# Kernel optimization log

Measured on AMD Instinct MI355X. Metric: run time of the kernel, lower is better.

Reference implementation:

```python
import jax, jax.numpy as jnp
import numpy as np

T = 8
TAU = 2.0       # spikingjelly LIFNode default tau
VTH = 1.0       # default v_threshold
ALPHA = 2.0     # surrogate.ATan alpha
EPS = 1e-5      # BatchNorm eps


@jax.custom_vjp
def spike_fn(x):
    # Heaviside with ATan surrogate gradient
    return (x >= 0.0).astype(x.dtype)

def _spike_fwd(x):
    return (x >= 0.0).astype(x.dtype), x

def _spike_bwd(x, g):
    sg = (ALPHA / 2.0) / (1.0 + (jnp.pi / 2.0 * ALPHA * x) ** 2)
    return (g * sg,)

spike_fn.defvjp(_spike_fwd, _spike_bwd)


def lif(x_seq):
    """Multi-step LIF over leading time axis. decay_input=True, hard reset to 0, detach_reset."""
    def step(v, x):
        v = v + (x - v) / TAU            # charge
        s = spike_fn(v - VTH)            # fire (surrogate grad)
        v = v * (1.0 - jax.lax.stop_gradient(s))  # detached hard reset to v_reset=0
        return v, s
    _, s_seq = jax.lax.scan(step, jnp.zeros_like(x_seq[0]), x_seq)
    return s_seq


def conv2d(x, w, b, stride):
    y = jax.lax.conv_general_dilated(x, w, (stride, stride), 'VALID',
                                     dimension_numbers=('NCHW', 'OIHW', 'NCHW'))
    return y + b[None, :, None, None]


def batchnorm(x, g, b):
    # training-mode BN over merged (T*B, H, W) axes, matching step_mode='m' BatchNorm2d
    m = x.mean((0, 2, 3), keepdims=True)
    v = x.var((0, 2, 3), keepdims=True)
    return g[None, :, None, None] * (x - m) * jax.lax.rsqrt(v + EPS) + b[None, :, None, None]


def setup_inputs() -> dict:
    key = jax.random.key(0)
    ks = jax.random.split(key, 12)
    def w_init(k, shape):
        fan_in = int(np.prod(shape[1:]))
        return jax.random.normal(k, shape, dtype=jnp.float32) / np.sqrt(fan_in)
    x = jax.random.normal(ks[0], (128, 4, 84, 84), dtype=jnp.float32)
    return {
        'x': x,
        'conv1_w': w_init(ks[1], (32, 4, 8, 8)),  'conv1_b': jnp.zeros((32,), jnp.float32),
        'bn1_g': jnp.ones((32,), jnp.float32),    'bn1_b': jnp.zeros((32,), jnp.float32),
        'conv2_w': w_init(ks[2], (64, 32, 4, 4)), 'conv2_b': jnp.zeros((64,), jnp.float32),
        'bn2_g': jnp.ones((64,), jnp.float32),    'bn2_b': jnp.zeros((64,), jnp.float32),
        'conv3_w': w_init(ks[3], (64, 64, 3, 3)), 'conv3_b': jnp.zeros((64,), jnp.float32),
        'bn3_g': jnp.ones((64,), jnp.float32),    'bn3_b': jnp.zeros((64,), jnp.float32),
        'fc1_w': w_init(ks[4], (512, 3136)),      'fc1_b': jnp.zeros((512,), jnp.float32),
        'fco_w': w_init(ks[5], (2, 512)),         'fco_b': jnp.zeros((2,), jnp.float32),
    }


def reference(x, conv1_w, conv1_b, bn1_g, bn1_b, conv2_w, conv2_b, bn2_g, bn2_b,
              conv3_w, conv3_b, bn3_g, bn3_b, fc1_w, fc1_b, fco_w, fco_b):
    B = x.shape[0]
    # replicate input over T timesteps; fold T into batch for conv/BN (step_mode='m')
    xs = jnp.broadcast_to(x, (T,) + x.shape).reshape((T * B,) + x.shape[1:])

    h = batchnorm(conv2d(xs, conv1_w, conv1_b, 4), bn1_g, bn1_b)   # [TB,32,20,20]
    s = lif(h.reshape((T, B) + h.shape[1:]))
    h = s.reshape((T * B,) + s.shape[2:])

    h = batchnorm(conv2d(h, conv2_w, conv2_b, 2), bn2_g, bn2_b)    # [TB,64,9,9]
    s = lif(h.reshape((T, B) + h.shape[1:]))
    h = s.reshape((T * B,) + s.shape[2:])

    h = batchnorm(conv2d(h, conv3_w, conv3_b, 1), bn3_g, bn3_b)    # [TB,64,7,7]
    s = lif(h.reshape((T, B) + h.shape[1:]))                        # [T,B,64,7,7]

    feat = s.reshape(T, B, -1)                                      # [T,B,3136]
    hid = lif(jnp.einsum('tbi,oi->tbo', feat, fc1_w) + fc1_b)       # [T,B,512]
    out_seq = jnp.einsum('tbo,ko->tbk', hid, fco_w) + fco_b         # [T,B,2]
    return out_seq.mean(0)                                          # [B,2]
```

## Files before the change

kernel.cpp:

```cpp
#include <hip/hip_runtime.h>
#include <cstdint>
#include <cstddef>

#define TT 8

#define E2_ELEMS (128*64*81)
#define E3_ELEMS (128*64*49)

typedef __attribute__((ext_vector_type(8))) short short8;
typedef __attribute__((ext_vector_type(4))) float f32x4;

__global__ void prep_all(const float* __restrict__ w1, const float* __restrict__ w2,
                         const float* __restrict__ w3, float* __restrict__ wT1,
                         __bf16* __restrict__ w2f, __bf16* __restrict__ w3f) {
  int i = blockIdx.x * 256 + threadIdx.x;
  if (i < 8192) {
    int oc = i >> 8, pos = i & 255;
    wT1[(oc >> 4) * 4096 + pos * 16 + (oc & 15)] = w1[oc * 256 + pos];
  } else if (i < 106496) {
    int v = i - 8192;
    int j    = v & 7;
    int oc   = (v >> 3) & 63;
    int quad = (v >> 9) & 3;
    int ksg  = (v >> 11) & 15;
    int term = v >> 15;
    int k = ksg * 32 + quad * 8 + j;
    int ci = k >> 4, kpos = k & 15;
    float w = w2[oc * 512 + ci * 16 + kpos];
    float hf = (float)(__bf16)w;
    float r1 = w - hf;
    float mf = (float)(__bf16)r1;
    float r2 = r1 - mf;
    w2f[v] = (term == 0) ? (__bf16)w : (term == 1) ? (__bf16)r1 : (__bf16)r2;
  } else if (i < 217088) {
    int v = i - 106496;
    int j    = v & 7;
    int oc   = (v >> 3) & 63;
    int quad = (v >> 9) & 3;
    int tk   = v >> 11;
    int term = tk / 18, kstep = tk % 18;
    int k = kstep * 32 + quad * 8 + j;
    int pos = k >> 6, ci = k & 63;
    float w = w3[oc * 576 + ci * 9 + pos];
    float hf = (float)(__bf16)w;
    float r1 = w - hf;
    float mf = (float)(__bf16)r1;
    float r2 = r1 - mf;
    w3f[v] = (term == 0) ? (__bf16)w : (term == 1) ? (__bf16)r1 : (__bf16)r2;
  }
}

__global__ __launch_bounds__(256) void prep_wff(const float* __restrict__ w,
                                                __bf16* __restrict__ wf) {
  __shared__ float tile[12544];
  int oc0 = blockIdx.x * 32;
  int ci0 = blockIdx.y * 8;
  int tid = threadIdx.x;
  for (int f = tid; f < 12544; f += 256) {
    int oc_l = f / 392, r = f - oc_l * 392;
    tile[f] = w[(size_t)(oc0 + oc_l) * 3136 + ci0 * 49 + r];
  }
  __syncthreads();
  int squad = (ci0 & 31) >> 3;
  int sadd  = ci0 >> 5;
  for (int g = tid; g < 1568; g += 256) {
    int pos = g >> 5, oc_l = g & 31;
    union { __bf16 h[8]; uint4 u; } T0, T1, T2;
    #pragma unroll
    for (int j = 0; j < 8; j++) {
      float wv = tile[oc_l * 392 + j * 49 + pos];
      float hf = (float)(__bf16)wv;
      float r1 = wv - hf;
      float mf = (float)(__bf16)r1;
      float r2 = r1 - mf;
      T0.h[j] = (__bf16)wv; T1.h[j] = (__bf16)r1; T2.h[j] = (__bf16)r2;
    }
    int s = pos * 2 + sadd;
    size_t b0 = (((size_t)s * 4 + squad) * 512 + oc0 + oc_l) * 8;
    *(uint4*)(wf + b0)               = T0.u;
    *(uint4*)(wf + b0 + 1605632)     = T1.u;
    *(uint4*)(wf + b0 + 3211264)     = T2.u;
  }
}

__global__ __launch_bounds__(128) void k_conv1(const float* __restrict__ x,
                                               const float* __restrict__ wT,
                                               const float* __restrict__ bias,
                                               float* __restrict__ out,
                                               float* __restrict__ pout) {
  __shared__ float xt[8064];
  int tid = threadIdx.x;
  int img = blockIdx.x >> 2;
  int q   = blockIdx.x & 3;
  int och = blockIdx.y;
  float4* dst = (float4*)xt;
  #pragma unroll
  for (int ci = 0; ci < 4; ci++) {
    const float4* s4 = (const float4*)(x + (size_t)img * 28224 + ci * 7056 + q * 1680);
    for (int i = tid; i < 504; i += 128) dst[ci * 504 + i] = s4[i];
  }
  __syncthreads();
  bool active = tid < 100;
  int oyl = tid / 20, ox = tid % 20;
  float acc[16];
  #pragma unroll
  for (int j = 0; j < 16; j++) acc[j] = 0.f;
  if (active) {
    int xb0 = oyl * 336 + ox * 4;
    const float* wh = wT + och * 4096;
    #pragma unroll 1
    for (int ci = 0; ci < 4; ci++) {
      #pragma unroll 1
      for (int ky = 0; ky < 8; ky++) {
        const float* xr = xt + ci * 2016 + xb0 + ky * 84;
        float4 xa  = *(const float4*)xr;
        float4 xbv = *(const float4*)(xr + 4);
        const float* wr = wh + (ci * 8 + ky) * 128;
        float xs[8] = {xa.x, xa.y, xa.z, xa.w, xbv.x, xbv.y, xbv.z, xbv.w};
        #pragma unroll
        for (int kx = 0; kx < 8; kx++) {
          #pragma unroll
          for (int j = 0; j < 16; j++)
            acc[j] = fmaf(xs[kx], wr[kx * 16 + j], acc[j]);
        }
      }
    }
  }
  __syncthreads();
  size_t obase = (size_t)img * 12800 + och * 6400 + (q * 5 + oyl) * 20 + ox;
  #pragma unroll
  for (int j = 0; j < 16; j++) {
    float v = 0.f;
    if (active) {
      v = acc[j] + bias[och * 16 + j];
      out[obase + j * 400] = v;
    }
    xt[j * 128 + tid] = v;
    xt[2048 + j * 128 + tid] = v * v;
  }
  __syncthreads();
  for (int off = 64; off > 0; off >>= 1) {
    if (tid < off) {
      #pragma unroll
      for (int j = 0; j < 16; j++) {
        xt[j * 128 + tid] += xt[j * 128 + tid + off];
        xt[2048 + j * 128 + tid] += xt[2048 + j * 128 + tid + off];
      }
    }
    __syncthreads();
  }
  if (tid < 16) {
    pout[(och * 16 + tid) * 512 + blockIdx.x] = xt[tid * 128];
    pout[16384 + (och * 16 + tid) * 512 + blockIdx.x] = xt[2048 + tid * 128];
  }
}

__global__ void k_bnfinal2(const float* __restrict__ pin, int sqoff, float n,
                           float* __restrict__ meanArr, float* __restrict__ rstdArr) {
  __shared__ float l0[256], l1[256];
  int c = blockIdx.x, tid = threadIdx.x;
  l0[tid] = pin[c * 512 + tid] + pin[c * 512 + tid + 256];
  l1[tid] = pin[sqoff + c * 512 + tid] + pin[sqoff + c * 512 + tid + 256];
  __syncthreads();
  for (int k = 128; k > 0; k >>= 1) {
    if (tid < k) { l0[tid] += l0[tid + k]; l1[tid] += l1[tid + k]; }
    __syncthreads();
  }
  if (tid == 0) {
    float m = l0[0] / n;
    float var = l1[0] / n - m * m;
    meanArr[c] = m;
    rstdArr[c] = rsqrtf(var + 1e-5f);
  }
}

__global__ void k_lif1b(const float* __restrict__ h, const float* __restrict__ mean,
                        const float* __restrict__ rstd, const float* __restrict__ g,
                        const float* __restrict__ bb, uint32_t* __restrict__ sout) {
  int idx = blockIdx.x * 256 + threadIdx.x;
  int ic = idx / 20;
  int ci = ic & 31;
  const float* hp = h + (size_t)idx * 20;
  float gm = g[ci], mm = mean[ci], rs = rstd[ci], bc = bb[ci];
  float xv[20];
  #pragma unroll
  for (int j4 = 0; j4 < 5; j4++) {
    float4 hv = ((const float4*)hp)[j4];
    xv[j4 * 4 + 0] = gm * (hv.x - mm) * rs + bc;
    xv[j4 * 4 + 1] = gm * (hv.y - mm) * rs + bc;
    xv[j4 * 4 + 2] = gm * (hv.z - mm) * rs + bc;
    xv[j4 * 4 + 3] = gm * (hv.w - mm) * rs + bc;
  }
  float v[20];
  #pragma unroll
  for (int j = 0; j < 20; j++) v[j] = 0.f;
  #pragma unroll
  for (int t = 0; t < TT; t++) {
    uint32_t w = 0;
    #pragma unroll
    for (int j = 0; j < 20; j++) {
      v[j] = v[j] + (xv[j] - v[j]) * 0.5f;
      uint32_t s = (v[j] >= 1.0f);
      w |= s << j;
      if (s) v[j] = 0.f;
    }
    sout[t * 81920 + idx] = w;
  }
}

template <int W, int NROW>
__global__ void k_lifb(const float* __restrict__ h, const float* __restrict__ mean,
                       const float* __restrict__ rstd, const float* __restrict__ g,
                       const float* __restrict__ bb, uint32_t* __restrict__ sout,
                       int E) {
  int idx = blockIdx.x * 256 + threadIdx.x;
  int bc = idx / NROW;
  int c = bc & 63;
  float gm = g[c], mm = mean[c], rs = rstd[c], bcn = bb[c];
  float v[W];
  #pragma unroll
  for (int j = 0; j < W; j++) v[j] = 0.f;
  int nword = 128 * 64 * NROW;
  #pragma unroll
  for (int t = 0; t < TT; t++) {
    const float* hp = h + (size_t)t * E + (size_t)idx * W;
    uint32_t w = 0;
    #pragma unroll
    for (int j = 0; j < W; j++) {
      float xv = gm * (hp[j] - mm) * rs + bcn;
      v[j] = v[j] + (xv - v[j]) * 0.5f;
      uint32_t s = (v[j] >= 1.0f);
      w |= s << j;
      if (s) v[j] = 0.f;
    }
    sout[t * nword + idx] = w;
  }
}

__global__ __launch_bounds__(256) void k_conv2m(const uint32_t* __restrict__ s1b,
                                                const __bf16* __restrict__ wf,
                                                const float* __restrict__ bias,
                                                float* __restrict__ out,
                                                float* __restrict__ pout) {
  __shared__ uint32_t sp[1280];
  __shared__ uint4 wl4[3072];
  __bf16* wl = (__bf16*)wl4;
  int tid = threadIdx.x;
  int img0 = blockIdx.x * 2;
  {
    const uint32_t* src = s1b + (size_t)img0 * 640;
    for (int i = tid; i < 1280; i += 256) sp[i] = src[i];
  }
  int wave = tid >> 6, lane = tid & 63;
  int img_local = wave >> 1;
  int tg = wave & 1;
  int l15 = lane & 15, quad = lane >> 4;
  int ci_off = quad >> 1;
  int kyp = (quad & 1) * 2;
  int spb[3], sh[3];
  #pragma unroll
  for (int mt = 0; mt < 3; mt++) {
    int px = tg * 48 + mt * 16 + l15;
    if (px > 80) px = 80;
    int oy = px / 9, ox = px - oy * 9;
    sh[mt]  = ox * 2;
    spb[mt] = img_local * 640 + ci_off * 20 + oy * 2 + kyp;
  }
  f32x4 acc[3][4];
  #pragma unroll
  for (int mt = 0; mt < 3; mt++)
    #pragma unroll
    for (int nt = 0; nt < 4; nt++) acc[mt][nt] = (f32x4){0.f, 0.f, 0.f, 0.f};

  for (int kc = 0; kc < 4; kc++) {
    __syncthreads();
    for (int o = tid * 8; o < 24576; o += 2048) {
      int tk = o >> 11;
      int term = tk >> 2, ksl = tk & 3;
      const __bf16* src = wf + (((term * 16 + kc * 4 + ksl)) << 11) + (o & 2047);
      *(uint4*)(wl + o) = *(const uint4*)src;
    }
    __syncthreads();
    #pragma unroll
    for (int ks = 0; ks < 4; ks++) {
      int ksg = kc * 4 + ks;
      short8 a[3];
      #pragma unroll
      for (int mt = 0; mt < 3; mt++) {
        uint32_t w0 = sp[spb[mt] + ksg * 40];
        uint32_t w1 = sp[spb[mt] + ksg * 40 + 1];
        uint32_t n0 = (w0 >> sh[mt]) & 15u;
        uint32_t n1 = (w1 >> sh[mt]) & 15u;
        union { uint32_t u[4]; short8 v; } A;
        A.u[0] = ((n0 & 1u) ? 0x3F80u : 0u) | ((n0 & 2u) ? 0x3F800000u : 0u);
        A.u[1] = ((n0 & 4u) ? 0x3F80u : 0u) | ((n0 & 8u) ? 0x3F800000u : 0u);
        A.u[2] = ((n1 & 1u) ? 0x3F80u : 0u) | ((n1 & 2u) ? 0x3F800000u : 0u);
        A.u[3] = ((n1 & 4u) ? 0x3F80u : 0u) | ((n1 & 8u) ? 0x3F800000u : 0u);
        a[mt] = A.v;
      }
      #pragma unroll
      for (int term = 0; term < 3; term++) {
        int fb = ((term * 4 + ks) << 11) + (quad << 9);
        #pragma unroll
        for (int nt = 0; nt < 4; nt++) {
          short8 b = *(const short8*)(wl + fb + ((nt << 4) + l15) * 8);
          #pragma unroll
          for (int mt = 0; mt < 3; mt++)
            acc[mt][nt] = __builtin_amdgcn_mfma_f32_16x16x32_bf16(a[mt], b, acc[mt][nt], 0, 0, 0);
        }
      }
    }
  }
  float sl[4], sl2[4];
  #pragma unroll
  for (int nt = 0; nt < 4; nt++) {
    sl[nt] = 0.f; sl2[nt] = 0.f;
    int oc = nt * 16 + l15;
    float bv = bias[oc];
    float* op = out + ((size_t)(img0 + img_local) * 64 + oc) * 81;
    #pragma unroll
    for (int mt = 0; mt < 3; mt++) {
      int pxr = tg * 48 + mt * 16 + quad * 4;
      #pragma unroll
      for (int r = 0; r < 4; r++) {
        int px = pxr + r;
        if (px < 81) {
          float v = acc[mt][nt][r] + bv;
          op[px] = v;
          sl[nt] += v; sl2[nt] += v * v;
        }
      }
    }
  }
  __syncthreads();
  float* sred = (float*)wl4;
  #pragma unroll
  for (int nt = 0; nt < 4; nt++) {
    int idx = (nt * 16 + l15) * 16 + (wave * 4 + quad);
    sred[idx] = sl[nt];
    sred[1024 + idx] = sl2[nt];
  }
  __syncthreads();
  if (tid < 64) {
    float s = 0.f, s2 = 0.f;
    #pragma unroll
    for (int k = 0; k < 16; k++) { s += sred[tid * 16 + k]; s2 += sred[1024 + tid * 16 + k]; }
    pout[tid * 512 + blockIdx.x] = s;
    pout[32768 + tid * 512 + blockIdx.x] = s2;
  }
}

__global__ void k_s2T(const uint32_t* __restrict__ sbits, uint32_t* __restrict__ s2T) {
  __shared__ uint32_t sb[576];
  int n = blockIdx.x;
  int t = n >> 7, b = n & 127;
  int tid = threadIdx.x;
  const uint32_t* src = sbits + t * 73728 + b * 576;
  for (int i = tid; i < 576; i += 256) sb[i] = src[i];
  __syncthreads();
  if (tid >= 162) return;
  int half = tid & 1, pc = tid >> 1;
  int r = pc / 9, cpix = pc - r * 9;
  uint32_t w = 0;
  #pragma unroll
  for (int ci = 0; ci < 32; ci++)
    w |= (((sb[(half * 32 + ci) * 9 + r] >> cpix) & 1u) << ci);
  s2T[(size_t)n * 162 + pc * 2 + half] = w;
}

__global__ __launch_bounds__(256) void k_conv3m(const uint32_t* __restrict__ s2T,
                                                const __bf16* __restrict__ wf,
                                                const float* __restrict__ bias,
                                                float* __restrict__ out,
                                                float* __restrict__ pout) {
  __shared__ uint32_t sp[324];
  __shared__ uint4 wl4[4608];
  __bf16* wl = (__bf16*)wl4;
  int tid = threadIdx.x;
  int img0 = blockIdx.x * 2;
  {
    const uint32_t* src = s2T + (size_t)img0 * 162;
    for (int i = tid; i < 324; i += 256) sp[i] = src[i];
  }
  int wave = tid >> 6, lane = tid & 63;
  int img_local = wave >> 1, tg = wave & 1;
  int l15 = lane & 15, quad = lane >> 4;
  int qsh = quad * 8;
  int base[2];
  #pragma unroll
  for (int mt = 0; mt < 2; mt++) {
    int px = tg * 32 + mt * 16 + l15;
    if (px > 48) px = 48;
    int oy = px / 7, ox = px - oy * 7;
    base[mt] = img_local * 162 + (oy * 9 + ox) * 2;
  }
  f32x4 acc[2][4];
  #pragma unroll
  for (int mt = 0; mt < 2; mt++)
    #pragma unroll
    for (int nt = 0; nt < 4; nt++) acc[mt][nt] = (f32x4){0.f, 0.f, 0.f, 0.f};

  #pragma unroll
  for (int kc = 0; kc < 3; kc++) {
    __syncthreads();
    #pragma unroll
    for (int it = 0; it < 18; it++) {
      const __bf16* s = wf + (((it / 6) * 18 + kc * 6 + (it % 6)) << 11) + tid * 8;
      *(uint4*)(wl + (it << 11) + tid * 8) = *(const uint4*)s;
    }
    __syncthreads();
    #pragma unroll
    for (int ksl = 0; ksl < 6; ksl++) {
      int kstep = kc * 6 + ksl;
      int pos = kstep >> 1, cihalf = kstep & 1;
      int ky = pos / 3, kx = pos % 3;
      short8 a[2];
      #pragma unroll
      for (int mt = 0; mt < 2; mt++) {
        uint32_t word = sp[base[mt] + (ky * 9 + kx) * 2 + cihalf];
        uint32_t byt = (word >> qsh) & 255u;
        union { uint32_t u[4]; short8 v; } A;
        A.u[0] = ((byt & 1u)  ? 0x3F80u : 0u) | ((byt & 2u)   ? 0x3F800000u : 0u);
        A.u[1] = ((byt & 4u)  ? 0x3F80u : 0u) | ((byt & 8u)   ? 0x3F800000u : 0u);
        A.u[2] = ((byt & 16u) ? 0x3F80u : 0u) | ((byt & 32u)  ? 0x3F800000u : 0u);
        A.u[3] = ((byt & 64u) ? 0x3F80u : 0u) | ((byt & 128u) ? 0x3F800000u : 0u);
        a[mt] = A.v;
      }
      #pragma unroll
      for (int term = 0; term < 3; term++) {
        int fb = ((term * 6 + ksl) << 11) + (quad << 9);
        #pragma unroll
        for (int nt = 0; nt < 4; nt++) {
          short8 b = *(const short8*)(wl + fb + ((nt << 4) + l15) * 8);
          #pragma unroll
          for (int mt = 0; mt < 2; mt++)
            acc[mt][nt] = __builtin_amdgcn_mfma_f32_16x16x32_bf16(a[mt], b, acc[mt][nt], 0, 0, 0);
        }
      }
    }
  }
  float sl[4], sl2[4];
  #pragma unroll
  for (int nt = 0; nt < 4; nt++) {
    sl[nt] = 0.f; sl2[nt] = 0.f;
    int oc = nt * 16 + l15;
    float bv = bias[oc];
    float* op = out + ((size_t)(img0 + img_local) * 64 + oc) * 49;
    #pragma unroll
    for (int mt = 0; mt < 2; mt++) {
      int pxr = tg * 32 + mt * 16 + quad * 4;
      #pragma unroll
      for (int r = 0; r < 4; r++) {
        int px = pxr + r;
        if (px < 49) {
          float v = acc[mt][nt][r] + bv;
          op[px] = v;
          sl[nt] += v; sl2[nt] += v * v;
        }
      }
    }
  }
  __syncthreads();
  float* sred = (float*)wl4;
  #pragma unroll
  for (int nt = 0; nt < 4; nt++) {
    int idx = (nt * 16 + l15) * 16 + (wave * 4 + quad);
    sred[idx] = sl[nt];
    sred[1024 + idx] = sl2[nt];
  }
  __syncthreads();
  if (tid < 64) {
    float s = 0.f, s2 = 0.f;
    #pragma unroll
    for (int k = 0; k < 16; k++) { s += sred[tid * 16 + k]; s2 += sred[1024 + tid * 16 + k]; }
    pout[tid * 512 + blockIdx.x] = s;
    pout[32768 + tid * 512 + blockIdx.x] = s2;
  }
}

__global__ void k_s3T(const uint32_t* __restrict__ sbits, uint32_t* __restrict__ s3T) {
  __shared__ uint32_t sb[896];
  int r0 = blockIdx.x * 2;
  int tid = threadIdx.x;
  for (int i = tid; i < 896; i += 256) {
    int rl = i / 448, o = i - rl * 448;
    int row = r0 + rl;
    sb[i] = sbits[(row >> 7) * 57344 + (row & 127) * 448 + o];
  }
  __syncthreads();
  if (tid >= 196) return;
  int rl = tid / 98, k = tid - rl * 98;
  int pos = k >> 1, half = k & 1;
  int py = pos / 7, px = pos - py * 7;
  const uint32_t* base = sb + rl * 448 + half * 224 + py;
  uint32_t w = 0;
  #pragma unroll
  for (int ci = 0; ci < 32; ci++)
    w |= ((base[ci * 7] >> px) & 1u) << ci;
  s3T[(size_t)(r0 + rl) * 98 + k] = w;
}

__global__ __launch_bounds__(256) void k_fc1m(const uint32_t* __restrict__ s3T,
                                              const __bf16* __restrict__ wf,
                                              float* __restrict__ part) {
  __shared__ uint32_t aS[6272];
  int tid = threadIdx.x;
  int row0 = blockIdx.x * 64;
  int oc0  = blockIdx.y * 32;
  {
    const uint32_t* src = s3T + (size_t)row0 * 98;
    for (int i = tid; i < 6272; i += 256) aS[i] = src[i];
  }
  __syncthreads();
  int wave = tid >> 6, lane = tid & 63;
  int l15 = lane & 15, quad = lane >> 4;
  int qsh = quad * 8;
  f32x4 acc[4][2];
  #pragma unroll
  for (int mt = 0; mt < 4; mt++)
    #pragma unroll
    for (int nt = 0; nt < 2; nt++) acc[mt][nt] = (f32x4){0.f, 0.f, 0.f, 0.f};
  int nIter = (wave < 2) ? 25 : 24;
  #pragma unroll 1
  for (int i = 0; i < nIter; i++) {
    int ks = i * 4 + wave;
    short8 a[4];
    #pragma unroll
    for (int mt = 0; mt < 4; mt++) {
      uint32_t word = aS[(mt * 16 + l15) * 98 + ks];
      uint32_t byt = (word >> qsh) & 255u;
      union { uint32_t u[4]; short8 v; } A;
      A.u[0] = ((byt & 1u)  ? 0x3F80u : 0u) | ((byt & 2u)   ? 0x3F800000u : 0u);
      A.u[1] = ((byt & 4u)  ? 0x3F80u : 0u) | ((byt & 8u)   ? 0x3F800000u : 0u);
      A.u[2] = ((byt & 16u) ? 0x3F80u : 0u) | ((byt & 32u)  ? 0x3F800000u : 0u);
      A.u[3] = ((byt & 64u) ? 0x3F80u : 0u) | ((byt & 128u) ? 0x3F800000u : 0u);
      a[mt] = A.v;
    }
    #pragma unroll
    for (int term = 0; term < 3; term++) {
      size_t fb = ((size_t)((term * 98 + ks) * 4 + quad) * 512 + oc0 + l15) * 8;
      #pragma unroll
      for (int nt = 0; nt < 2; nt++) {
        short8 b = *(const short8*)(wf + fb + nt * 128);
        #pragma unroll
        for (int mt = 0; mt < 4; mt++)
          acc[mt][nt] = __builtin_amdgcn_mfma_f32_16x16x32_bf16(a[mt], b, acc[mt][nt], 0, 0, 0);
      }
    }
  }
  #pragma unroll
  for (int mt = 0; mt < 4; mt++) {
    #pragma unroll
    for (int nt = 0; nt < 2; nt++) {
      int oc = oc0 + nt * 16 + l15;
      #pragma unroll
      for (int r = 0; r < 4; r++) {
        int row = row0 + mt * 16 + quad * 4 + r;
        part[(size_t)wave * 524288 + (size_t)row * 512 + oc] = acc[mt][nt][r];
      }
    }
  }
}

__global__ void k_fc1red_lif(const float* __restrict__ part, const float* __restrict__ bias,
                             unsigned char* __restrict__ hid) {
  int idx = blockIdx.x * 256 + threadIdx.x;
  float bv = bias[idx & 511];
  float v = 0.f;
  #pragma unroll
  for (int t = 0; t < TT; t++) {
    float a = part[t * 65536 + idx];
    #pragma unroll
    for (int j = 1; j < 4; j++) a += part[(size_t)j * 524288 + t * 65536 + idx];
    a += bv;
    v = v + (a - v) * 0.5f;
    unsigned char s = (v >= 1.0f);
    hid[t * 65536 + idx] = s;
    if (s) v = 0.f;
  }
}

__global__ void k_fco(const unsigned char* __restrict__ hid, const float* __restrict__ w,
                      const float* __restrict__ bias, float* __restrict__ out) {
  int b = blockIdx.x, tid = threadIdx.x;
  float a0 = 0.f, a1 = 0.f;
  for (int t = 0; t < TT; t++) {
    const unsigned char* hrow = hid + ((size_t)t * 128 + b) * 512;
    for (int o = tid; o < 512; o += 256) {
      if (hrow[o]) { a0 += w[o]; a1 += w[512 + o]; }
    }
  }
  __shared__ float l0[256], l1[256];
  l0[tid] = a0; l1[tid] = a1; __syncthreads();
  for (int k = 128; k > 0; k >>= 1) {
    if (tid < k) { l0[tid] += l0[tid + k]; l1[tid] += l1[tid + k]; }
    __syncthreads();
  }
  if (tid == 0) {
    out[b * 2 + 0] = l0[0] * 0.125f + bias[0];
    out[b * 2 + 1] = l1[0] * 0.125f + bias[1];
  }
}

extern "C" void kernel_launch(void* const* d_in, const int* in_sizes, int n_in,
                              void* d_out, int out_size, void* d_ws, size_t ws_size,
                              hipStream_t stream) {
  const float* x    = (const float*)d_in[0];
  const float* c1w  = (const float*)d_in[1];
  const float* c1b  = (const float*)d_in[2];
  const float* bn1g = (const float*)d_in[3];
  const float* bn1b = (const float*)d_in[4];
  const float* c2w  = (const float*)d_in[5];
  const float* c2b  = (const float*)d_in[6];
  const float* bn2g = (const float*)d_in[7];
  const float* bn2b = (const float*)d_in[8];
  const float* c3w  = (const float*)d_in[9];
  const float* c3b  = (const float*)d_in[10];
  const float* bn3g = (const float*)d_in[11];
  const float* bn3b = (const float*)d_in[12];
  const float* fc1w = (const float*)d_in[13];
  const float* fc1b = (const float*)d_in[14];
  const float* fcow = (const float*)d_in[15];
  const float* fcob = (const float*)d_in[16];
  float* out = (float*)d_out;

  char* ws = (char*)d_ws;
  float*    h1     = (float*)(ws + 0);
  uint32_t* s1bits = (uint32_t*)(ws + 6553600);
  float*    h2     = (float*)(ws + 19660800);
  uint32_t* s2bits = (uint32_t*)(ws + 40894464);
  float*    h3     = (float*)(ws + 46202880);
  uint32_t* s3bits = (uint32_t*)(ws + 59047936);
  unsigned char* hid = (unsigned char*)(ws + 64356352);
  float*    st     = (float*)(ws + 64880640);
  __bf16*   w2f  = (__bf16*)(ws + 60882944);
  __bf16*   w3f  = (__bf16*)(ws + 61079552);
  uint32_t* s2T  = (uint32_t*)(ws + 61300736);
  float*    wT1  = (float*)(ws + 62390272);
  float*    bnpart = (float*)(ws + 9437184);
  __bf16*   wff    = (__bf16*)(ws + 19660800);
  float*    f1part = (float*)(ws + 29360128);
  uint32_t* s3T    = (uint32_t*)(ws + 43253760);

  prep_all   <<<848, 256, 0, stream>>>(c1w, c2w, c3w, wT1, w2f, w3f);
  k_conv1    <<<dim3(512, 2), 128, 0, stream>>>(x, wT1, c1b, h1, bnpart);
  k_bnfinal2 <<<32, 256, 0, stream>>>(bnpart, 16384, 51200.f, st, st + 32);
  k_lif1b    <<<320, 256, 0, stream>>>(h1, st, st + 32, bn1g, bn1b, s1bits);

  k_conv2m   <<<512, 256, 0, stream>>>(s1bits, w2f, c2b, h2, bnpart);
  k_bnfinal2 <<<64, 256, 0, stream>>>(bnpart, 32768, 82944.f, st + 64, st + 128);
  k_lifb<9, 9><<<288, 256, 0, stream>>>(h2, st + 64, st + 128, bn2g, bn2b, s2bits, E2_ELEMS);
  prep_wff   <<<dim3(16, 8), 256, 0, stream>>>(fc1w, wff);

  k_s2T      <<<1024, 256, 0, stream>>>(s2bits, s2T);
  k_conv3m   <<<512, 256, 0, stream>>>(s2T, w3f, c3b, h3, bnpart);
  k_bnfinal2 <<<64, 256, 0, stream>>>(bnpart, 32768, 50176.f, st + 192, st + 256);
  k_lifb<7, 7><<<224, 256, 0, stream>>>(h3, st + 192, st + 256, bn3g, bn3b, s3bits, E3_ELEMS);

  k_s3T      <<<512, 256, 0, stream>>>(s3bits, s3T);
  k_fc1m     <<<dim3(16, 16), 256, 0, stream>>>(s3T, wff, f1part);
  k_fc1red_lif<<<256, 256, 0, stream>>>(f1part, fc1b, hid);
  k_fco      <<<128, 256, 0, stream>>>(hid, fcow, fcob, out);
}
```

Before: 260.8 us.

## Fuse LIF with bit transposes and fc1 LIF with output layer; split conv waves by channels

The layer-2 and layer-3 LIF kernels are fused with the bit-transpose kernels, so spike bitmasks go through shared memory straight into the transposed layout and never round-trip through a global intermediate. The fc1 reduction+LIF is fused with the output projection, which removes the hid buffer and one launch. In conv2/conv3 each wave now covers all pixels for half the output channels instead of half the pixels for all channels, which changes the A/B register reuse balance. The workspace is re-laid out to avoid overlap. The fused LIF kernels use only 256 blocks with a serial time loop and barriers, which may lower parallelism.

New measurement: 250.4 us (median of 2 runs). 4.0% less time.

```diff
diff --git a/kernel.cpp b/kernel.cpp
--- a/kernel.cpp
+++ b/kernel.cpp
@@ -77,9 +77,9 @@
     }
     int s = pos * 2 + sadd;
     size_t b0 = (((size_t)s * 4 + squad) * 512 + oc0 + oc_l) * 8;
-    *(uint4*)(wf + b0)               = T0.u;
-    *(uint4*)(wf + b0 + 1605632)     = T1.u;
-    *(uint4*)(wf + b0 + 3211264)     = T2.u;
+    *(uint4*)(wf + b0)           = T0.u;
+    *(uint4*)(wf + b0 + 1605632) = T1.u;
+    *(uint4*)(wf + b0 + 3211264) = T2.u;
   }
 }
 
@@ -208,35 +208,6 @@
   }
 }
 
-template <int W, int NROW>
-__global__ void k_lifb(const float* __restrict__ h, const float* __restrict__ mean,
-                       const float* __restrict__ rstd, const float* __restrict__ g,
-                       const float* __restrict__ bb, uint32_t* __restrict__ sout,
-                       int E) {
-  int idx = blockIdx.x * 256 + threadIdx.x;
-  int bc = idx / NROW;
-  int c = bc & 63;
-  float gm = g[c], mm = mean[c], rs = rstd[c], bcn = bb[c];
-  float v[W];
-  #pragma unroll
-  for (int j = 0; j < W; j++) v[j] = 0.f;
-  int nword = 128 * 64 * NROW;
-  #pragma unroll
-  for (int t = 0; t < TT; t++) {
-    const float* hp = h + (size_t)t * E + (size_t)idx * W;
-    uint32_t w = 0;
-    #pragma unroll
-    for (int j = 0; j < W; j++) {
-      float xv = gm * (hp[j] - mm) * rs + bcn;
-      v[j] = v[j] + (xv - v[j]) * 0.5f;
-      uint32_t s = (v[j] >= 1.0f);
-      w |= s << j;
-      if (s) v[j] = 0.f;
-    }
-    sout[t * nword + idx] = w;
-  }
-}
-
 __global__ __launch_bounds__(256) void k_conv2m(const uint32_t* __restrict__ s1b,
                                                 const __bf16* __restrict__ wf,
                                                 const float* __restrict__ bias,
@@ -253,24 +224,24 @@
   }
   int wave = tid >> 6, lane = tid & 63;
   int img_local = wave >> 1;
-  int tg = wave & 1;
+  int nh = wave & 1;
   int l15 = lane & 15, quad = lane >> 4;
   int ci_off = quad >> 1;
   int kyp = (quad & 1) * 2;
-  int spb[3], sh[3];
-  #pragma unroll
-  for (int mt = 0; mt < 3; mt++) {
-    int px = tg * 48 + mt * 16 + l15;
+  int spb[6], sh[6];
+  #pragma unroll
+  for (int mt = 0; mt < 6; mt++) {
+    int px = mt * 16 + l15;
     if (px > 80) px = 80;
     int oy = px / 9, ox = px - oy * 9;
     sh[mt]  = ox * 2;
     spb[mt] = img_local * 640 + ci_off * 20 + oy * 2 + kyp;
   }
-  f32x4 acc[3][4];
-  #pragma unroll
-  for (int mt = 0; mt < 3; mt++)
-    #pragma unroll
-    for (int nt = 0; nt < 4; nt++) acc[mt][nt] = (f32x4){0.f, 0.f, 0.f, 0.f};
+  f32x4 acc[6][2];
+  #pragma unroll
+  for (int mt = 0; mt < 6; mt++)
+    #pragma unroll
+    for (int nt = 0; nt < 2; nt++) acc[mt][nt] = (f32x4){0.f, 0.f, 0.f, 0.f};
 
   for (int kc = 0; kc < 4; kc++) {
     __syncthreads();
@@ -284,9 +255,9 @@
     #pragma unroll
     for (int ks = 0; ks < 4; ks++) {
       int ksg = kc * 4 + ks;
-      short8 a[3];
-      #pragma unroll
-      for (int mt = 0; mt < 3; mt++) {
+      short8 a[6];
+      #pragma unroll
+      for (int mt = 0; mt < 6; mt++) {
         uint32_t w0 = sp[spb[mt] + ksg * 40];
         uint32_t w1 = sp[spb[mt] + ksg * 40 + 1];
         uint32_t n0 = (w0 >> sh[mt]) & 15u;
@@ -302,25 +273,25 @@
       for (int term = 0; term < 3; term++) {
         int fb = ((term * 4 + ks) << 11) + (quad << 9);
         #pragma unroll
-        for (int nt = 0; nt < 4; nt++) {
-          short8 b = *(const short8*)(wl + fb + ((nt << 4) + l15) * 8);
+        for (int nt = 0; nt < 2; nt++) {
+          short8 b = *(const short8*)(wl + fb + ((((nh << 1) | nt) << 4) + l15) * 8);
           #pragma unroll
-          for (int mt = 0; mt < 3; mt++)
+          for (int mt = 0; mt < 6; mt++)
             acc[mt][nt] = __builtin_amdgcn_mfma_f32_16x16x32_bf16(a[mt], b, acc[mt][nt], 0, 0, 0);
         }
       }
     }
   }
-  float sl[4], sl2[4];
-  #pragma unroll
-  for (int nt = 0; nt < 4; nt++) {
+  float sl[2], sl2[2];
+  #pragma unroll
+  for (int nt = 0; nt < 2; nt++) {
     sl[nt] = 0.f; sl2[nt] = 0.f;
-    int oc = nt * 16 + l15;
+    int oc = nh * 32 + nt * 16 + l15;
     float bv = bias[oc];
     float* op = out + ((size_t)(img0 + img_local) * 64 + oc) * 81;
     #pragma unroll
-    for (int mt = 0; mt < 3; mt++) {
-      int pxr = tg * 48 + mt * 16 + quad * 4;
+    for (int mt = 0; mt < 6; mt++) {
+      int pxr = mt * 16 + quad * 4;
       #pragma unroll
       for (int r = 0; r < 4; r++) {
         int px = pxr + r;
@@ -335,37 +306,79 @@
   __syncthreads();
   float* sred = (float*)wl4;
   #pragma unroll
-  for (int nt = 0; nt < 4; nt++) {
-    int idx = (nt * 16 + l15) * 16 + (wave * 4 + quad);
+  for (int nt = 0; nt < 2; nt++) {
+    int oc = nh * 32 + nt * 16 + l15;
+    int idx = oc * 8 + img_local * 4 + quad;
     sred[idx] = sl[nt];
-    sred[1024 + idx] = sl2[nt];
+    sred[512 + idx] = sl2[nt];
   }
   __syncthreads();
   if (tid < 64) {
     float s = 0.f, s2 = 0.f;
     #pragma unroll
-    for (int k = 0; k < 16; k++) { s += sred[tid * 16 + k]; s2 += sred[1024 + tid * 16 + k]; }
+    for (int k = 0; k < 8; k++) { s += sred[tid * 8 + k]; s2 += sred[512 + tid * 8 + k]; }
     pout[tid * 512 + blockIdx.x] = s;
     pout[32768 + tid * 512 + blockIdx.x] = s2;
   }
 }
 
-__global__ void k_s2T(const uint32_t* __restrict__ sbits, uint32_t* __restrict__ s2T) {
-  __shared__ uint32_t sb[576];
-  int n = blockIdx.x;
-  int t = n >> 7, b = n & 127;
+__global__ __launch_bounds__(256) void k_lifb2T(const float* __restrict__ h,
+                                                const float* __restrict__ mean,
+                                                const float* __restrict__ rstd,
+                                                const float* __restrict__ g,
+                                                const float* __restrict__ bb,
+                                                uint32_t* __restrict__ s2T) {
+  __shared__ uint32_t sb[288];
+  int b = blockIdx.x, half = blockIdx.y;
   int tid = threadIdx.x;
-  const uint32_t* src = sbits + t * 73728 + b * 576;
-  for (int i = tid; i < 576; i += 256) sb[i] = src[i];
-  __syncthreads();
-  if (tid >= 162) return;
-  int half = tid & 1, pc = tid >> 1;
-  int r = pc / 9, cpix = pc - r * 9;
-  uint32_t w = 0;
-  #pragma unroll
-  for (int ci = 0; ci < 32; ci++)
-    w |= (((sb[(half * 32 + ci) * 9 + r] >> cpix) & 1u) << ci);
-  s2T[(size_t)n * 162 + pc * 2 + half] = w;
+  int c1 = half * 32 + tid / 9, py1 = tid % 9;
+  bool has2 = tid < 32;
+  int r2 = tid + 256;
+  int c2i = half * 32 + r2 / 9, py2 = r2 % 9;
+  float gm1 = g[c1], mm1 = mean[c1], rs1 = rstd[c1], bc1 = bb[c1];
+  float gm2 = 0.f, mm2 = 0.f, rs2 = 0.f, bc2 = 0.f;
+  if (has2) { gm2 = g[c2i]; mm2 = mean[c2i]; rs2 = rstd[c2i]; bc2 = bb[c2i]; }
+  float v1[9], v2[9];
+  #pragma unroll
+  for (int j = 0; j < 9; j++) { v1[j] = 0.f; v2[j] = 0.f; }
+  size_t base1 = ((size_t)b * 64 + c1) * 81 + py1 * 9;
+  size_t base2 = has2 ? ((size_t)b * 64 + c2i) * 81 + py2 * 9 : base1;
+  #pragma unroll 1
+  for (int t = 0; t < TT; t++) {
+    const float* hp = h + (size_t)t * E2_ELEMS;
+    uint32_t w = 0;
+    #pragma unroll
+    for (int j = 0; j < 9; j++) {
+      float xv = gm1 * (hp[base1 + j] - mm1) * rs1 + bc1;
+      v1[j] = v1[j] + (xv - v1[j]) * 0.5f;
+      uint32_t s = (v1[j] >= 1.0f);
+      w |= s << j;
+      if (s) v1[j] = 0.f;
+    }
+    sb[tid] = w;
+    if (has2) {
+      uint32_t w2 = 0;
+      #pragma unroll
+      for (int j = 0; j < 9; j++) {
+        float xv = gm2 * (hp[base2 + j] - mm2) * rs2 + bc2;
+        v2[j] = v2[j] + (xv - v2[j]) * 0.5f;
+        uint32_t s = (v2[j] >= 1.0f);
+        w2 |= s << j;
+        if (s) v2[j] = 0.f;
+      }
+      sb[r2] = w2;
+    }
+    __syncthreads();
+    if (tid < 81) {
+      int r = tid / 9, cpix = tid - r * 9;
+      uint32_t wo = 0;
+      #pragma unroll
+      for (int ci = 0; ci < 32; ci++)
+        wo |= ((sb[ci * 9 + r] >> cpix) & 1u) << ci;
+      s2T[(size_t)(t * 128 + b) * 162 + tid * 2 + half] = wo;
+    }
+    __syncthreads();
+  }
 }
 
 __global__ __launch_bounds__(256) void k_conv3m(const uint32_t* __restrict__ s2T,
@@ -383,22 +396,22 @@
     for (int i = tid; i < 324; i += 256) sp[i] = src[i];
   }
   int wave = tid >> 6, lane = tid & 63;
-  int img_local = wave >> 1, tg = wave & 1;
+  int img_local = wave >> 1, nh = wave & 1;
   int l15 = lane & 15, quad = lane >> 4;
   int qsh = quad * 8;
-  int base[2];
-  #pragma unroll
-  for (int mt = 0; mt < 2; mt++) {
-    int px = tg * 32 + mt * 16 + l15;
+  int base[4];
+  #pragma unroll
+  for (int mt = 0; mt < 4; mt++) {
+    int px = mt * 16 + l15;
     if (px > 48) px = 48;
     int oy = px / 7, ox = px - oy * 7;
     base[mt] = img_local * 162 + (oy * 9 + ox) * 2;
   }
-  f32x4 acc[2][4];
-  #pragma unroll
-  for (int mt = 0; mt < 2; mt++)
-    #pragma unroll
-    for (int nt = 0; nt < 4; nt++) acc[mt][nt] = (f32x4){0.f, 0.f, 0.f, 0.f};
+  f32x4 acc[4][2];
+  #pragma unroll
+  for (int mt = 0; mt < 4; mt++)
+    #pragma unroll
+    for (int nt = 0; nt < 2; nt++) acc[mt][nt] = (f32x4){0.f, 0.f, 0.f, 0.f};
 
   #pragma unroll
   for (int kc = 0; kc < 3; kc++) {
@@ -414,9 +427,9 @@
       int kstep = kc * 6 + ksl;
       int pos = kstep >> 1, cihalf = kstep & 1;
       int ky = pos / 3, kx = pos % 3;
-      short8 a[2];
-      #pragma unroll
-      for (int mt = 0; mt < 2; mt++) {
+      short8 a[4];
+      #pragma unroll
+      for (int mt = 0; mt < 4; mt++) {
         uint32_t word = sp[base[mt] + (ky * 9 + kx) * 2 + cihalf];
         uint32_t byt = (word >> qsh) & 255u;
         union { uint32_t u[4]; short8 v; } A;
@@ -430,25 +443,25 @@
       for (int term = 0; term < 3; term++) {
         int fb = ((term * 6 + ksl) << 11) + (quad << 9);
         #pragma unroll
-        for (int nt = 0; nt < 4; nt++) {
-          short8 b = *(const short8*)(wl + fb + ((nt << 4) + l15) * 8);
+        for (int nt = 0; nt < 2; nt++) {
+          short8 b = *(const short8*)(wl + fb + ((((nh << 1) | nt) << 4) + l15) * 8);
           #pragma unroll
-          for (int mt = 0; mt < 2; mt++)
+          for (int mt = 0; mt < 4; mt++)
             acc[mt][nt] = __builtin_amdgcn_mfma_f32_16x16x32_bf16(a[mt], b, acc[mt][nt], 0, 0, 0);
         }
       }
     }
   }
-  float sl[4], sl2[4];
-  #pragma unroll
-  for (int nt = 0; nt < 4; nt++) {
+  float sl[2], sl2[2];
+  #pragma unroll
+  for (int nt = 0; nt < 2; nt++) {
     sl[nt] = 0.f; sl2[nt] = 0.f;
-    int oc = nt * 16 + l15;
+    int oc = nh * 32 + nt * 16 + l15;
     float bv = bias[oc];
     float* op = out + ((size_t)(img0 + img_local) * 64 + oc) * 49;
     #pragma unroll
-    for (int mt = 0; mt < 2; mt++) {
-      int pxr = tg * 32 + mt * 16 + quad * 4;
+    for (int mt = 0; mt < 4; mt++) {
+      int pxr = mt * 16 + quad * 4;
       #pragma unroll
       for (int r = 0; r < 4; r++) {
         int px = pxr + r;
@@ -463,41 +476,65 @@
   __syncthreads();
   float* sred = (float*)wl4;
   #pragma unroll
-  for (int nt = 0; nt < 4; nt++) {
-    int idx = (nt * 16 + l15) * 16 + (wave * 4 + quad);
+  for (int nt = 0; nt < 2; nt++) {
+    int oc = nh * 32 + nt * 16 + l15;
+    int idx = oc * 8 + img_local * 4 + quad;
     sred[idx] = sl[nt];
-    sred[1024 + idx] = sl2[nt];
+    sred[512 + idx] = sl2[nt];
   }
   __syncthreads();
   if (tid < 64) {
     float s = 0.f, s2 = 0.f;
     #pragma unroll
-    for (int k = 0; k < 16; k++) { s += sred[tid * 16 + k]; s2 += sred[1024 + tid * 16 + k]; }
+    for (int k = 0; k < 8; k++) { s += sred[tid * 8 + k]; s2 += sred[512 + tid * 8 + k]; }
     pout[tid * 512 + blockIdx.x] = s;
     pout[32768 + tid * 512 + blockIdx.x] = s2;
   }
 }
 
-__global__ void k_s3T(const uint32_t* __restrict__ sbits, uint32_t* __restrict__ s3T) {
-  __shared__ uint32_t sb[896];
-  int r0 = blockIdx.x * 2;
+__global__ __launch_bounds__(256) void k_lifb3T(const float* __restrict__ h,
+                                                const float* __restrict__ mean,
+                                                const float* __restrict__ rstd,
+                                                const float* __restrict__ g,
+                                                const float* __restrict__ bb,
+                                                uint32_t* __restrict__ s3T) {
+  __shared__ uint32_t sb[224];
+  int b = blockIdx.x, half = blockIdx.y;
   int tid = threadIdx.x;
-  for (int i = tid; i < 896; i += 256) {
-    int rl = i / 448, o = i - rl * 448;
-    int row = r0 + rl;
-    sb[i] = sbits[(row >> 7) * 57344 + (row & 127) * 448 + o];
-  }
-  __syncthreads();
-  if (tid >= 196) return;
-  int rl = tid / 98, k = tid - rl * 98;
-  int pos = k >> 1, half = k & 1;
-  int py = pos / 7, px = pos - py * 7;
-  const uint32_t* base = sb + rl * 448 + half * 224 + py;
-  uint32_t w = 0;
-  #pragma unroll
-  for (int ci = 0; ci < 32; ci++)
-    w |= ((base[ci * 7] >> px) & 1u) << ci;
-  s3T[(size_t)(r0 + rl) * 98 + k] = w;
+  bool active = tid < 224;
+  int row = active ? tid : 0;
+  int c = half * 32 + row / 7, py = row % 7;
+  float gm = g[c], mm = mean[c], rs = rstd[c], bc = bb[c];
+  float v[7];
+  #pragma unroll
+  for (int j = 0; j < 7; j++) v[j] = 0.f;
+  size_t base = ((size_t)b * 64 + c) * 49 + py * 7;
+  #pragma unroll 1
+  for (int t = 0; t < TT; t++) {
+    const float* hp = h + (size_t)t * E3_ELEMS;
+    if (active) {
+      uint32_t w = 0;
+      #pragma unroll
+      for (int j = 0; j < 7; j++) {
+        float xv = gm * (hp[base + j] - mm) * rs + bc;
+        v[j] = v[j] + (xv - v[j]) * 0.5f;
+        uint32_t s = (v[j] >= 1.0f);
+        w |= s << j;
+        if (s) v[j] = 0.f;
+      }
+      sb[tid] = w;
+    }
+    __syncthreads();
+    if (tid < 49) {
+      int py2 = tid / 7, px = tid - py2 * 7;
+      uint32_t wo = 0;
+      #pragma unroll
+      for (int ci = 0; ci < 32; ci++)
+        wo |= ((sb[ci * 7 + py2] >> px) & 1u) << ci;
+      s3T[(size_t)(t * 128 + b) * 98 + tid * 2 + half] = wo;
+    }
+    __syncthreads();
+  }
 }
 
 __global__ __launch_bounds__(256) void k_fc1m(const uint32_t* __restrict__ s3T,
@@ -562,33 +599,36 @@
   }
 }
 
-__global__ void k_fc1red_lif(const float* __restrict__ part, const float* __restrict__ bias,
-                             unsigned char* __restrict__ hid) {
-  int idx = blockIdx.x * 256 + threadIdx.x;
-  float bv = bias[idx & 511];
-  float v = 0.f;
+__global__ __launch_bounds__(256) void k_fc1fco(const float* __restrict__ part,
+                                                const float* __restrict__ bias,
+                                                const float* __restrict__ w,
+                                                const float* __restrict__ fcob,
+                                                float* __restrict__ out) {
+  int b = blockIdx.x, tid = threadIdx.x;
+  int o0 = tid, o1 = tid + 256;
+  float bv0 = bias[o0], bv1 = bias[o1];
+  float v0 = 0.f, v1 = 0.f;
+  float a0 = 0.f, a1 = 0.f;
   #pragma unroll
   for (int t = 0; t < TT; t++) {
-    float a = part[t * 65536 + idx];
-    #pragma unroll
-    for (int j = 1; j < 4; j++) a += part[(size_t)j * 524288 + t * 65536 + idx];
-    a += bv;
-    v = v + (a - v) * 0.5f;
-    unsigned char s = (v >= 1.0f);
-    hid[t * 65536 + idx] = s;
-    if (s) v = 0.f;
-  }
-}
-
-__global__ void k_fco(const unsigned char* __restrict__ hid, const float* __restrict__ w,
-                      const float* __restrict__ bias, float* __restrict__ out) {
-  int b = blockIdx.x, tid = threadIdx.x;
-  float a0 = 0.f, a1 = 0.f;
-  for (int t = 0; t < TT; t++) {
-    const unsigned char* hrow = hid + ((size_t)t * 128 + b) * 512;
-    for (int o = tid; o < 512; o += 256) {
-      if (hrow[o]) { a0 += w[o]; a1 += w[512 + o]; }
-    }
+    int idx0 = t * 65536 + b * 512 + o0;
+    float s0 = part[idx0];
+    #pragma unroll
+    for (int j = 1; j < 4; j++) s0 += part[(size_t)j * 524288 + idx0];
+    s0 += bv0;
+    v0 = v0 + (s0 - v0) * 0.5f;
+    bool sp0 = (v0 >= 1.0f);
+    if (sp0) v0 = 0.f;
+    int idx1 = idx0 + 256;
+    float s1 = part[idx1];
+    #pragma unroll
+    for (int j = 1; j < 4; j++) s1 += part[(size_t)j * 524288 + idx1];
+    s1 += bv1;
+    v1 = v1 + (s1 - v1) * 0.5f;
+    bool sp1 = (v1 >= 1.0f);
+    if (sp1) v1 = 0.f;
+    if (sp0) { a0 += w[o0]; a1 += w[512 + o0]; }
+    if (sp1) { a0 += w[o1]; a1 += w[512 + o1]; }
   }
   __shared__ float l0[256], l1[256];
   l0[tid] = a0; l1[tid] = a1; __syncthreads();
@@ -597,8 +637,8 @@
     __syncthreads();
   }
   if (tid == 0) {
-    out[b * 2 + 0] = l0[0] * 0.125f + bias[0];
-    out[b * 2 + 1] = l1[0] * 0.125f + bias[1];
+    out[b * 2 + 0] = l0[0] * 0.125f + fcob[0];
+    out[b * 2 + 1] = l1[0] * 0.125f + fcob[1];
   }
 }
 
@@ -628,37 +668,31 @@
   float*    h1     = (float*)(ws + 0);
   uint32_t* s1bits = (uint32_t*)(ws + 6553600);
   float*    h2     = (float*)(ws + 19660800);
-  uint32_t* s2bits = (uint32_t*)(ws + 40894464);
   float*    h3     = (float*)(ws + 46202880);
-  uint32_t* s3bits = (uint32_t*)(ws + 59047936);
-  unsigned char* hid = (unsigned char*)(ws + 64356352);
+  __bf16*   w2f    = (__bf16*)(ws + 60882944);
+  __bf16*   w3f    = (__bf16*)(ws + 61079552);
+  uint32_t* s2T    = (uint32_t*)(ws + 61300736);
+  float*    wT1    = (float*)(ws + 62390272);
   float*    st     = (float*)(ws + 64880640);
-  __bf16*   w2f  = (__bf16*)(ws + 60882944);
-  __bf16*   w3f  = (__bf16*)(ws + 61079552);
-  uint32_t* s2T  = (uint32_t*)(ws + 61300736);
-  float*    wT1  = (float*)(ws + 62390272);
-  float*    bnpart = (float*)(ws + 9437184);
-  __bf16*   wff    = (__bf16*)(ws + 19660800);
-  float*    f1part = (float*)(ws + 29360128);
-  uint32_t* s3T    = (uint32_t*)(ws + 43253760);
+  __bf16*   wff    = (__bf16*)(ws + 67108864);
+  float*    f1part = (float*)(ws + 76742656);
+  uint32_t* s3T    = (uint32_t*)(ws + 85131264);
+  float*    bnpart = (float*)(ws + 85532672);
 
   prep_all   <<<848, 256, 0, stream>>>(c1w, c2w, c3w, wT1, w2f, w3f);
+  prep_wff   <<<dim3(16, 8), 256, 0, stream>>>(fc1w, wff);
   k_conv1    <<<dim3(512, 2), 128, 0, stream>>>(x, wT1, c1b, h1, bnpart);
   k_bnfinal2 <<<32, 256, 0, stream>>>(bnpart, 16384, 51200.f, st, st + 32);
   k_lif1b    <<<320, 256, 0, stream>>>(h1, st, st + 32, bn1g, bn1b, s1bits);
 
   k_conv2m   <<<512, 256, 0, stream>>>(s1bits, w2f, c2b, h2, bnpart);
   k_bnfinal2 <<<64, 256, 0, stream>>>(bnpart, 32768, 82944.f, st + 64, st + 128);
-  k_lifb<9, 9><<<288, 256, 0, stream>>>(h2, st + 64, st + 128, bn2g, bn2b, s2bits, E2_ELEMS);
-  prep_wff   <<<dim3(16, 8), 256, 0, stream>>>(fc1w, wff);
-
-  k_s2T      <<<1024, 256, 0, stream>>>(s2bits, s2T);
+  k_lifb2T   <<<dim3(128, 2), 256, 0, stream>>>(h2, st + 64, st + 128, bn2g, bn2b, s2T);
+
   k_conv3m   <<<512, 256, 0, stream>>>(s2T, w3f, c3b, h3, bnpart);
   k_bnfinal2 <<<64, 256, 0, stream>>>(bnpart, 32768, 50176.f, st + 192, st + 256);
-  k_lifb<7, 7><<<224, 256, 0, stream>>>(h3, st + 192, st + 256, bn3g, bn3b, s3bits, E3_ELEMS);
-
-  k_s3T      <<<512, 256, 0, stream>>>(s3bits, s3T);
+  k_lifb3T   <<<dim3(128, 2), 256, 0, stream>>>(h3, st + 192, st + 256, bn3g, bn3b, s3T);
+
   k_fc1m     <<<dim3(16, 16), 256, 0, stream>>>(s3T, wff, f1part);
-  k_fc1red_lif<<<256, 256, 0, stream>>>(f1part, fc1b, hid);
-  k_fco      <<<128, 256, 0, stream>>>(hid, fcow, fcob, out);
-}
+  k_fc1fco   <<<128, 256, 0, stream>>>(f1part, fc1b, fcow, fcob, out);
+}
```
